# Performance work log

Hardware: AMD Instinct MI355X
Metric: run time of the kernel (lower is better)

## Reference

```python
import jax, jax.numpy as jnp
import numpy as np

B, L, M, H, VN, VK = 128, 30, 10, 256, 32000, 2000
VT = VN + VK


def setup_inputs() -> dict:
    key = jax.random.key(0)
    ks = jax.random.split(key, 24)
    p = lambda k, shape: jax.random.normal(k, shape, jnp.float32) * 0.02
    eye = jnp.eye(H, dtype=jnp.float32)
    return {
        "sentence": jax.random.randint(ks[0], (B, L, 1), 0, VN),
        "keywords": jax.random.randint(ks[1], (B, M, 1), VN, VT),
        "categories": jax.random.randint(ks[2], (B, M, 1), VN, VT),
        "memory_size": jax.random.randint(ks[3], (B,), 1, M + 1),
        "use_teacher_forcing": 1,
        "emb": p(ks[4], (VT, H)),
        "W_ct": p(ks[5], (H, 5 * H)), "b_ct": jnp.zeros((H,), jnp.float32),
        "W_ih": p(ks[6], (4 * H, H)), "W_hh": p(ks[7], (4 * H, H)),
        "b_ih": jnp.zeros((4 * H,), jnp.float32), "b_hh": jnp.zeros((4 * H,), jnp.float32),
        "W_n": eye + p(ks[8], (H, H)), "W_k": eye + p(ks[9], (H, H)), "W_v": eye + p(ks[10], (H, H)),
        "W_nv": p(ks[11], (VN, H)), "b_nv": jnp.zeros((VN,), jnp.float32),
        "W_g": p(ks[12], (1, H)), "b_g": jnp.zeros((1,), jnp.float32),
        "W_hn": p(ks[13], (L, (L + 1) * H)), "b_hn": jnp.zeros((L,), jnp.float32),
        "W_hk": p(ks[14], (L, (L + 1) * H)), "b_hk": jnp.zeros((L,), jnp.float32),
        "W_hv": p(ks[15], (L, (L + 1) * H)), "b_hv": jnp.zeros((L,), jnp.float32),
        "W_mk": p(ks[16], (M, 4 * H)), "b_mk": jnp.zeros((M,), jnp.float32),
        "W_mv": p(ks[17], (M, 4 * H)), "b_mv": jnp.zeros((M,), jnp.float32),
    }


def _forward(sentence, keywords, categories, memory_size, use_teacher_forcing,
             emb, W_ct, b_ct, W_ih, W_hh, b_ih, b_hh, W_n, W_k, W_v,
             W_nv, b_nv, W_g, b_g, W_hn, b_hn, W_hk, b_hk, W_hv, b_hv,
             W_mk, b_mk, W_mv, b_mv):
    # prepare_memory: embed keyword/category ids, zero rows past memory_size
    ke = emb[keywords[:, :, 0]]      # (B,M,H)
    ve = emb[categories[:, :, 0]]    # (B,M,H)
    mask = (jnp.arange(M)[None, :] < memory_size[:, None])[..., None].astype(emb.dtype)
    key_mem = ke * mask
    val_mem = ve * mask
    ms = memory_size.astype(emb.dtype)[:, None]
    # prepare_history: initial hidden = (avg_mk + avg_mv)/2 at t=0
    init_h = (key_mem.sum(1) + val_mem.sum(1)) / (2.0 * ms)  # (B,H)
    hist0 = jnp.zeros((B, L, H), emb.dtype).at[:, 0, :].set(init_h)

    toks = sentence[:, 1:, 0].T          # (L-1, B) teacher tokens
    dis = jnp.arange(1, L)

    def step(carry, xs):
        histN, histK, histV, prev_h, prev_emb, loss = carry
        di, tok = xs

        def attn_h(hist, W, b):
            q = jnp.concatenate([prev_h, hist.reshape(B, -1)], axis=1)  # (B,(L+1)H)
            w = jnp.tanh(q @ W.T + b)                                    # (B,L)
            return jnp.einsum('bl,blh->bh', w, hist)

        cHN = attn_h(histN, W_hn, b_hn)
        cHK = attn_h(histK, W_hk, b_hk)
        cHV = attn_h(histV, W_hv, b_hv)
        cH = jnp.concatenate([cHN, cHK, cHV], axis=1)  # (B,3H)
        q_m = jnp.concatenate([prev_h, cH], axis=1)    # (B,4H)

        def attn_m(mem, W, b):
            w = jnp.tanh(q_m @ W.T + b)                # (B,M)
            return jnp.einsum('bm,bmh->bh', w, mem)

        cMK = attn_m(key_mem, W_mk, b_mk)
        cMV = attn_m(val_mem, W_mv, b_mv)
        # W_Ct_reshape(cat 5H) -> LSTM initial cell state
        c0 = jnp.concatenate([cH, cMK, cMV], axis=1) @ W_ct.T + b_ct  # (B,H)
        # single-step LSTM (torch gate order i,f,g,o)
        gates = prev_emb @ W_ih.T + b_ih + prev_h @ W_hh.T + b_hh
        gi, gf, gg, go = jnp.split(gates, 4, axis=1)
        c = jax.nn.sigmoid(gf) * c0 + jax.nn.sigmoid(gi) * jnp.tanh(gg)
        h = jax.nn.sigmoid(go) * jnp.tanh(c)           # (B,H)

        hN = h @ W_n.T
        hK = h @ W_k.T
        hV = h @ W_v.T
        histN = histN.at[:, di, :].set(hN)
        histK = histK.at[:, di, :].set(hK)
        histV = histV.at[:, di, :].set(hV)

        P_N = jax.nn.softmax(hN @ W_nv.T + b_nv, axis=1)                       # (B,VN)
        P_MK = jax.nn.softmax(jnp.einsum('bmh,bh->bm', key_mem, hK), axis=1)   # (B,M)
        P_MV = jax.nn.softmax(jnp.einsum('bmh,bh->bm', val_mem, hV), axis=1)
        P_M = 0.5 * (P_MK + P_MV)
        gt = jax.nn.sigmoid(h @ W_g.T + b_g)           # (B,1)
        P = jnp.concatenate([P_N * gt, P_M * (1.0 - gt)], axis=1)
        p_tok = jnp.take_along_axis(P, tok[:, None], axis=1)[:, 0]
        loss = loss - jnp.log(p_tok).sum()
        prev_emb = emb[tok]                            # teacher forcing
        return (histN, histK, histV, h, prev_emb, loss), gt

    carry0 = (hist0, hist0, hist0, init_h, emb[sentence[:, 0, 0]],
              jnp.zeros((), emb.dtype))
    carry, gs = jax.lax.scan(step, carry0, (dis, toks))
    loss = carry[5]
    g_history = jnp.zeros((B, L, 1), emb.dtype).at[:, 1:, :].set(
        jnp.transpose(gs, (1, 0, 2)))
    return loss, g_history


def reference(sentence, keywords, categories, memory_size, use_teacher_forcing,
              emb, W_ct, b_ct, W_ih, W_hh, b_ih, b_hh, W_n, W_k, W_v,
              W_nv, b_nv, W_g, b_g, W_hn, b_hn, W_hk, b_hk, W_hv, b_hv,
              W_mk, b_mk, W_mv, b_mv):
    return _forward(sentence, keywords, categories, memory_size, use_teacher_forcing,
                    emb, W_ct, b_ct, W_ih, W_hh, b_ih, b_hh, W_n, W_k, W_v,
                    W_nv, b_nv, W_g, b_g, W_hn, b_hn, W_hk, b_hk, W_hv, b_hv,
                    W_mk, b_mk, W_mv, b_mv)
```

## Files before the change

### kernel.cpp

```cpp
#include <hip/hip_runtime.h>
#include <math.h>

#define B_ 128
#define L_ 30
#define M_ 10
#define H_ 256
#define VN_ 32000
#define NCHK 500
#define NG 3712

typedef __bf16 bf16;
typedef bf16 bf16x8 __attribute__((ext_vector_type(8)));
typedef float f32x4 __attribute__((ext_vector_type(4)));

#define MFMA(a,b,c) __builtin_amdgcn_mfma_f32_16x16x32_bf16(a, b, c, 0, 0, 0)

__device__ __forceinline__ float rcpf(float x) { return __builtin_amdgcn_rcpf(x); }
__device__ __forceinline__ float sigf(float x) { return rcpf(1.f + __expf(-x)); }
__device__ __forceinline__ float ftanh(float x) {
  float e = __expf(2.f * x);
  return 1.f - 2.f * rcpf(e + 1.f);
}
__device__ __forceinline__ float u2lo(unsigned w) { return __builtin_bit_cast(float, w << 16); }
__device__ __forceinline__ float u2hi(unsigned w) { return __builtin_bit_cast(float, w & 0xffff0000u); }
__device__ __forceinline__ unsigned packbf2(float a, float b) {
  unsigned short lo = __builtin_bit_cast(unsigned short, (bf16)a);
  unsigned short hi = __builtin_bit_cast(unsigned short, (bf16)b);
  return (unsigned)lo | ((unsigned)hi << 16);
}

#if __has_builtin(__builtin_amdgcn_fdot2_f32_bf16)
typedef __bf16 bf16x2 __attribute__((ext_vector_type(2)));
__device__ __forceinline__ float dot2(unsigned x, unsigned w, float c) {
  return __builtin_amdgcn_fdot2_f32_bf16(__builtin_bit_cast(bf16x2, x),
                                         __builtin_bit_cast(bf16x2, w), c, false);
}
#else
__device__ __forceinline__ float dot2(unsigned x, unsigned w, float c) {
  c = fmaf(u2lo(x), u2lo(w), c);
  return fmaf(u2hi(x), u2hi(w), c);
}
#endif

__global__ __launch_bounds__(256) void k_prep(
    const float* W_ct, const float* W_hh,
    const float* W_n, const float* W_k, const float* W_v,
    const float* W_hn, const float* W_hk, const float* W_hv,
    const float* W_mk, const float* W_mv, const float* W_g,
    unsigned* WhhP, unsigned* WnkvP, unsigned* WctPH, unsigned* WctP45,
    unsigned* WmP0, unsigned* WmPQ, unsigned* WhdA, unsigned* WhdB, unsigned* WgP) {
  int stride = gridDim.x * blockDim.x;
  int base = blockIdx.x * blockDim.x + threadIdx.x;
  for (int i = base; i < 131072; i += stride) {
    int k2 = i >> 10, n = i & 1023;
    WhhP[i] = packbf2(W_hh[n*256 + 2*k2], W_hh[n*256 + 2*k2 + 1]);
  }
  for (int i = base; i < 98304; i += stride) {
    int k2 = i / 768, n = i - (i/768)*768;
    const float* s = (n < 256) ? W_n : (n < 512) ? W_k : W_v;
    int nn = n & 255;
    WnkvP[i] = packbf2(s[nn*256 + 2*k2], s[nn*256 + 2*k2 + 1]);
  }
  for (int i = base; i < 98304; i += stride) {
    int X = i >> 15, r = i & 32767, k2 = r >> 8, n = r & 255;
    int col = X*256 + 2*k2;
    WctPH[i] = packbf2(W_ct[n*1280 + col], W_ct[n*1280 + col + 1]);
  }
  for (int i = base; i < 65536; i += stride) {
    int X = i >> 15, r = i & 32767, k2 = r >> 8, n = r & 255;
    int col = 768 + X*256 + 2*k2;
    WctP45[i] = packbf2(W_ct[n*1280 + col], W_ct[n*1280 + col + 1]);
  }
  for (int i = base; i < 4096; i += stride) {
    int k2 = i >> 5, c = i & 31;
    float x0 = 0.f, x1 = 0.f;
    if (c < 10)              { x0 = W_mk[c*1024 + 2*k2]; x1 = W_mk[c*1024 + 2*k2 + 1]; }
    else if (c >= 16 && c < 26) { int m = c-16; x0 = W_mv[m*1024 + 2*k2]; x1 = W_mv[m*1024 + 2*k2 + 1]; }
    WmP0[i] = packbf2(x0, x1);
  }
  for (int i = base; i < 12288; i += stride) {
    int X = i >> 12, r = i & 4095, k2 = r >> 5, c = r & 31;
    int off = 256 + X*256 + 2*k2;
    float x0 = 0.f, x1 = 0.f;
    if (c < 10)              { x0 = W_mk[c*1024 + off]; x1 = W_mk[c*1024 + off + 1]; }
    else if (c >= 16 && c < 26) { int m = c-16; x0 = W_mv[m*1024 + off]; x1 = W_mv[m*1024 + off + 1]; }
    WmPQ[i] = packbf2(x0, x1);
  }
  for (int i = base; i < 491520; i += stride) {
    int d = i >> 14, r = i & 16383, k2 = r >> 7, c = r & 127;
    float x0 = 0.f, x1 = 0.f;
    if (c < 96) {
      int X = c >> 5, l = c & 31;
      if (l < 30) {
        const float* W = (X == 0) ? W_hn : (X == 1) ? W_hk : W_hv;
        x0 = W[l*7936 + d*256 + 2*k2]; x1 = W[l*7936 + d*256 + 2*k2 + 1];
      }
    }
    WhdA[i] = packbf2(x0, x1);
  }
  for (int i = base; i < 16384; i += stride) {
    int k2 = i >> 7, c = i & 127;
    float x0 = 0.f, x1 = 0.f;
    if (c < 96) {
      int X = c >> 5, l = c & 31;
      if (l < 30) {
        const float* W = (X == 0) ? W_hn : (X == 1) ? W_hk : W_hv;
        x0 = W[l*7936 + 2*k2]; x1 = W[l*7936 + 2*k2 + 1];
      }
    }
    WhdB[i] = packbf2(x0, x1);
  }
  for (int i = base; i < 128; i += stride) WgP[i] = packbf2(W_g[2*i], W_g[2*i+1]);
}

__global__ __launch_bounds__(256) void k_pregates(
    const int* sentence, const float* emb, const float* W_ih,
    const float* b_ih, const float* b_hh, float* prehg) {
  extern __shared__ char smp[];
  char* Al = smp;
  char* Bl = smp + 65536;
  __shared__ int tok_s[128];
  int blk = blockIdx.x;
  int gd = blk >> 3, nc = blk & 7;
  int t = threadIdx.x, wid = t >> 6, lane = t & 63;
  if (t < 128) tok_s[t] = sentence[t*L_ + gd];
  __syncthreads();
  for (int i = t; i < 128*32; i += 256) {
    int r = i >> 5, c8 = i & 31;
    const float* e = emb + (size_t)tok_s[r]*H_ + c8*8;
    float4 f0 = *(const float4*)e, f1 = *(const float4*)(e + 4);
    int4 v;
    v.x = (int)packbf2(f0.x, f0.y); v.y = (int)packbf2(f0.z, f0.w);
    v.z = (int)packbf2(f1.x, f1.y); v.w = (int)packbf2(f1.z, f1.w);
    *(int4*)(Al + ((r*512 + c8*16) ^ ((r&7)<<4))) = v;
    const float* wsrc = W_ih + (size_t)(nc*128 + r)*H_ + c8*8;
    float4 g0 = *(const float4*)wsrc, g1 = *(const float4*)(wsrc + 4);
    int4 w;
    w.x = (int)packbf2(g0.x, g0.y); w.y = (int)packbf2(g0.z, g0.w);
    w.z = (int)packbf2(g1.x, g1.y); w.w = (int)packbf2(g1.z, g1.w);
    *(int4*)(Bl + ((r*512 + c8*16) ^ ((r&7)<<4))) = w;
  }
  __syncthreads();
  f32x4 acc[2][8] = {};
  #pragma unroll 2
  for (int kk = 0; kk < 8; ++kk) {
    int kb2 = kk*64 + (lane>>4)*16;
    bf16x8 af[2], bfr[8];
    #pragma unroll
    for (int fi = 0; fi < 2; ++fi) {
      int m = wid*32 + fi*16 + (lane & 15);
      af[fi] = *(const bf16x8*)(Al + ((m*512 + kb2) ^ ((m&7)<<4)));
    }
    #pragma unroll
    for (int fj = 0; fj < 8; ++fj) {
      int n = fj*16 + (lane & 15);
      bfr[fj] = *(const bf16x8*)(Bl + ((n*512 + kb2) ^ ((n&7)<<4)));
    }
    #pragma unroll
    for (int fi = 0; fi < 2; ++fi)
      #pragma unroll
      for (int fj = 0; fj < 8; ++fj)
        acc[fi][fj] = MFMA(af[fi], bfr[fj], acc[fi][fj]);
  }
  #pragma unroll
  for (int fi = 0; fi < 2; ++fi)
    #pragma unroll
    for (int fj = 0; fj < 8; ++fj)
      #pragma unroll
      for (int r = 0; r < 4; ++r) {
        int row = wid*32 + fi*16 + (lane>>4)*4 + r;
        int col = nc*128 + fj*16 + (lane & 15);
        prehg[((size_t)gd*128 + row)*1024 + col] = acc[fi][fj][r] + b_ih[col] + b_hh[col];
      }
}

struct LoopP {
  const int *sentence, *keywords, *categories, *memsz;
  const float *emb;
  const unsigned *WhhP, *WnkvP, *WctPH, *WctP45, *WmP0, *WmPQ, *WhdA, *WhdB, *WgP;
  const float *prehg;
  const float *b_ct, *b_hn, *b_hk, *b_hv, *b_mk, *b_mv, *b_g;
  unsigned* hNb;
  unsigned* hNbT;
  float* gt_all;
  float* outg;
};

__global__ __launch_bounds__(1024) void k_loop(LoopP p) {
  extern __shared__ unsigned Su[];
  float* Sf = (float*)Su;
  const int t = threadIdx.x, b = blockIdx.x;
  enum { PH = 0,
         QM = 11520,
         P45 = 14400,
         MB = 16960,
         GA = 19520,
         HP = 20544,
         HV = 20672,
         SW = 21056, ACA = 21152, SWM = 21248, M0 = 21280,
         DA = 21312, DB = 21440,
         BCT = 21568, BH = 21824, BM = 21920, BG = 21952 };

  for (int i = t; i < 2560; i += 1024) {
    int X = i / 1280, r = i - X*1280, m = r >> 7, j = r & 127;
    int ms = p.memsz[b];
    int idx = (X == 0 ? p.keywords : p.categories)[b*M_ + m];
    unsigned u = 0;
    if (m < ms) {
      const float* e = p.emb + (size_t)idx*H_ + 2*j;
      u = packbf2(e[0], e[1]);
    }
    Su[MB + i] = u;
  }
  if (t < 256) Sf[BCT + t] = p.b_ct[t];
  if (t < 96) {
    int X = t >> 5, l = t & 31;
    const float* bh = (X == 0) ? p.b_hn : (X == 1) ? p.b_hk : p.b_hv;
    Sf[BH + t] = (l < 30) ? bh[l] : 0.f;
    Sf[ACA + t] = 0.f;
  }
  if (t < 32) {
    float v = 0.f;
    if (t < 10) v = p.b_mk[t];
    else if (t >= 16 && t < 26) v = p.b_mv[t - 16];
    Sf[BM + t] = v;
  }
  if (t == 0) { Sf[BG] = p.b_g[0]; p.outg[b*L_] = 0.f; }
  __syncthreads();
  if (t < 128) {
    float a0 = 0.f, a1 = 0.f;
    #pragma unroll
    for (int q = 0; q < 20; ++q) {
      unsigned u = Su[MB + q*128 + t];
      a0 += u2lo(u); a1 += u2hi(u);
    }
    float msf = (float)p.memsz[b];
    unsigned up = packbf2(a0 / (2.f * msf), a1 / (2.f * msf));
    Su[HP + t] = up;
    Su[HV + t] = up; Su[HV + 128 + t] = up; Su[HV + 256 + t] = up;
  }
  for (int q = t; q < 2560; q += 1024) {
    int X = q / 1280, r = q - X*1280, m = r >> 7, j = r & 127;
    float a0 = 0.f, a1 = 0.f;
    const uint2* wp = (const uint2*)(p.WctP45 + (X << 15)) + j;
    const unsigned* mb = Su + MB + X*1280 + m*128;
    #pragma unroll 4
    for (int k2 = 0; k2 < 128; ++k2) {
      uint2 w = wp[k2 << 7];
      unsigned u = mb[k2];
      a0 = dot2(u, w.x, a0);
      a1 = dot2(u, w.y, a1);
    }
    Su[P45 + q] = packbf2(a0, a1);
  }
  __syncthreads();

  for (int di = 1; di < L_; ++di) {
    {
      const float pre = p.prehg[(size_t)(((di-1) << 7) | b)*1024 + t];
      float e0 = 0.f, e1 = 0.f;
      const unsigned* wp = p.WhhP + t;
      #pragma unroll 8
      for (int k2 = 0; k2 < 128; k2 += 2) {
        e0 = dot2(Su[HP + k2],     wp[k2 << 10],     e0);
        e1 = dot2(Su[HP + k2 + 1], wp[(k2+1) << 10], e1);
      }
      Sf[GA + t] = pre + e0 + e1;
    }
    if (t < 128) {
      float a = 0.f;
      const unsigned* wp = p.WhdA + ((size_t)di << 14) + t;
      const unsigned* hv = Su + HV + ((t >> 5) << 7);
      #pragma unroll 8
      for (int k2 = 0; k2 < 128; ++k2) a = dot2(hv[k2 & 127], wp[k2 << 7], a);
      Sf[DA + t] = a;
    } else if (t < 256) {
      int c = t - 128;
      float a = 0.f;
      const unsigned* wp = p.WhdB + c;
      #pragma unroll 8
      for (int k2 = 0; k2 < 128; ++k2) a = dot2(Su[HP + k2], wp[k2 << 7], a);
      Sf[DB + c] = a;
    } else if (t < 640) {
      int q = t - 256, X = q >> 7, j = q & 127;
      float a0 = 0.f, a1 = 0.f;
      const unsigned* hv = Su + HV + (X << 7);
      const uint2* wp = (const uint2*)(p.WctPH + (X << 15)) + j;
      #pragma unroll 4
      for (int k2 = 0; k2 < 128; ++k2) {
        uint2 w = wp[k2 << 7];
        a0 = dot2(hv[k2], w.x, a0);
        a1 = dot2(hv[k2], w.y, a1);
      }
      Su[PH + (X*30 + di-1)*128 + j] = packbf2(a0, a1);
    } else if (t < 736) {
      int q = t - 640, X = q >> 5, c = q & 31;
      float a = 0.f;
      const unsigned* wp = p.WmPQ + (X << 12) + c;
      const unsigned* hv = Su + HV + (X << 7);
      #pragma unroll 8
      for (int k2 = 0; k2 < 128; ++k2) a = dot2(hv[k2], wp[k2 << 5], a);
      Sf[QM + (X*30 + di-1)*32 + c] = a;
    } else if (t >= 768 && t < 800) {
      int c = t - 768;
      float a = 0.f;
      const unsigned* wp = p.WmP0 + c;
      #pragma unroll 8
      for (int k2 = 0; k2 < 128; ++k2) a = dot2(Su[HP + k2], wp[k2 << 5], a);
      Sf[M0 + c] = a;
    }
    __syncthreads();
    if (t < 96) {
      float a = Sf[ACA + t] + Sf[DA + t];
      Sf[ACA + t] = a;
      Sf[SW + t] = ftanh(a + Sf[DB + t] + Sf[BH + t]);
    }
    __syncthreads();
    if (t < 32) {
      bool valid = (t < 10) || (t >= 16 && t < 26);
      if (valid) {
        float aN = 0.f, aK = 0.f, aV = 0.f;
        const float* sw0 = Sf + SW;
        const float* q0 = Sf + QM + t;
        for (int l = 0; l < di; ++l) {
          aN = fmaf(sw0[l],      q0[l*32],        aN);
          aK = fmaf(sw0[32 + l], q0[960 + l*32],  aK);
          aV = fmaf(sw0[64 + l], q0[1920 + l*32], aV);
        }
        Sf[SWM + t] = ftanh(Sf[M0 + t] + Sf[BM + t] + aN + aK + aV);
      }
    }
    __syncthreads();
    if (t < 128) {
      float a0 = Sf[BCT + 2*t], a1 = Sf[BCT + 2*t + 1];
      for (int X = 0; X < 3; ++X) {
        const float* swp = Sf + SW + X*32;
        const unsigned* php = Su + PH + X*3840 + t;
        float e0 = 0.f, e1 = 0.f, o0 = 0.f, o1 = 0.f;
        int l = 0;
        for (; l + 1 < di; l += 2) {
          float s0 = swp[l], s1 = swp[l+1];
          unsigned ua = php[l*128], ub = php[(l+1)*128];
          e0 = fmaf(s0, u2lo(ua), e0); e1 = fmaf(s0, u2hi(ua), e1);
          o0 = fmaf(s1, u2lo(ub), o0); o1 = fmaf(s1, u2hi(ub), o1);
        }
        if (l < di) {
          float s = swp[l]; unsigned u = php[l*128];
          e0 = fmaf(s, u2lo(u), e0); e1 = fmaf(s, u2hi(u), e1);
        }
        a0 += e0 + o0; a1 += e1 + o1;
      }
      {
        float p0 = 0.f, p1 = 0.f, q0 = 0.f, q1 = 0.f;
        #pragma unroll
        for (int m = 0; m < 10; ++m) {
          float sk = Sf[SWM + m], sv = Sf[SWM + 16 + m];
          unsigned uk = Su[P45 + m*128 + t], uv = Su[P45 + 1280 + m*128 + t];
          p0 = fmaf(sk, u2lo(uk), p0); p1 = fmaf(sk, u2hi(uk), p1);
          q0 = fmaf(sv, u2lo(uv), q0); q1 = fmaf(sv, u2hi(uv), q1);
        }
        a0 += p0 + q0; a1 += p1 + q1;
      }
      int n0 = 2*t;
      float gi0 = Sf[GA+n0],   gf0 = Sf[GA+256+n0], gg0 = Sf[GA+512+n0], go0 = Sf[GA+768+n0];
      float gi1 = Sf[GA+n0+1], gf1 = Sf[GA+257+n0], gg1 = Sf[GA+513+n0], go1 = Sf[GA+769+n0];
      float cc0 = sigf(gf0)*a0 + sigf(gi0)*ftanh(gg0);
      float cc1 = sigf(gf1)*a1 + sigf(gi1)*ftanh(gg1);
      float h0 = sigf(go0)*ftanh(cc0);
      float h1 = sigf(go1)*ftanh(cc1);
      Su[HP + t] = packbf2(h0, h1);
    }
    __syncthreads();
    if (t < 384) {
      int X = t >> 7, j = t & 127;
      float a0 = 0.f, a1 = 0.f;
      const uint2* wp = (const uint2*)p.WnkvP + t;
      #pragma unroll 4
      for (int k2 = 0; k2 < 128; ++k2) {
        uint2 w = wp[k2*384];
        unsigned u = Su[HP + k2];
        a0 = dot2(u, w.x, a0);
        a1 = dot2(u, w.y, a1);
      }
      unsigned up = packbf2(a0, a1);
      Su[HV + t] = up;
      if (X == 0) {
        int tile = di - 1;
        p.hNb[(size_t)((tile << 7) | b)*128 + j] = up;
        int idx = ((((tile*4 + (b>>5))*8 + (j>>4))*64 + ((j>>2)&3)*16 + (b&15))*2 + ((b>>4)&1))*4 + (j&3);
        p.hNbT[idx] = up;
      }
    } else if (t >= 448 && t < 512) {
      int j = t - 448;
      float a = dot2(Su[HP + 2*j], p.WgP[2*j], 0.f);
      a = dot2(Su[HP + 2*j + 1], p.WgP[2*j + 1], a);
      #pragma unroll
      for (int o = 1; o < 64; o <<= 1) a += __shfl_xor(a, o);
      if (j == 0) {
        float g = sigf(a + Sf[BG]);
        p.gt_all[((di-1) << 7) | b] = g;
        p.outg[b*L_ + di] = g;
      }
    }
    __syncthreads();
  }
}

__global__ __launch_bounds__(256) void k_vocab(
    const unsigned* hNbT, const float* W_nv, const float* b_nv, float2* pmps) {
  extern __shared__ char smv[];
  int ch = blockIdx.x;
  int t = threadIdx.x, wid = t >> 6, lane = t & 63;
  int v0 = ch * 64;
  for (int i = t; i < 64*32; i += 256) {
    int r = i >> 5, c8 = i & 31;
    const float* wsrc = W_nv + (size_t)(v0 + r)*H_ + c8*8;
    float4 f0 = *(const float4*)wsrc, f1 = *(const float4*)(wsrc + 4);
    int4 v;
    v.x = (int)packbf2(f0.x, f0.y); v.y = (int)packbf2(f0.z, f0.w);
    v.z = (int)packbf2(f1.x, f1.y); v.w = (int)packbf2(f1.z, f1.w);
    *(int4*)(smv + ((r*512 + c8*16) ^ ((r&7)<<4))) = v;
  }
  float bb4[4];
  #pragma unroll
  for (int fj = 0; fj < 4; ++fj) bb4[fj] = b_nv[v0 + fj*16 + (lane & 15)];
  __syncthreads();
  const int4* At = (const int4*)hNbT;
  for (int tile = 0; tile < 29; ++tile) {
    f32x4 acc[2][4] = {};
    #pragma unroll 2
    for (int kk = 0; kk < 8; ++kk) {
      int kb2 = kk*64 + (lane>>4)*16;
      bf16x8 af[2], bfr[4];
      #pragma unroll
      for (int fi = 0; fi < 2; ++fi) {
        int4 u = At[((tile*4 + wid)*8 + kk)*128 + lane*2 + fi];
        af[fi] = __builtin_bit_cast(bf16x8, u);
      }
      #pragma unroll
      for (int fj = 0; fj < 4; ++fj) {
        int n = fj*16 + (lane & 15);
        bfr[fj] = *(const bf16x8*)(smv + ((n*512 + kb2) ^ ((n&7)<<4)));
      }
      #pragma unroll
      for (int fi = 0; fi < 2; ++fi)
        #pragma unroll
        for (int fj = 0; fj < 4; ++fj)
          acc[fi][fj] = MFMA(af[fi], bfr[fj], acc[fi][fj]);
    }
    #pragma unroll
    for (int fi = 0; fi < 2; ++fi)
      #pragma unroll
      for (int r = 0; r < 4; ++r) {
        float mi = acc[fi][0][r] + bb4[0];
        #pragma unroll
        for (int fj = 1; fj < 4; ++fj) mi = fmaxf(mi, acc[fi][fj][r] + bb4[fj]);
        for (int o = 1; o < 16; o <<= 1) mi = fmaxf(mi, __shfl_xor(mi, o));
        float si = 0.f;
        #pragma unroll
        for (int fj = 0; fj < 4; ++fj) si += __expf(acc[fi][fj][r] + bb4[fj] - mi);
        for (int o = 1; o < 16; o <<= 1) si += __shfl_xor(si, o);
        if ((lane & 15) == 0) {
          int row = wid*32 + fi*16 + (lane>>4)*4 + r;
          pmps[(size_t)ch*NG + tile*128 + row] = make_float2(mi, si);
        }
      }
  }
}

__global__ __launch_bounds__(128) void k_combine(
    const float2* pmps, const unsigned* hNb, const float* W_nv, const float* b_nv,
    const float* gt_all, const int* sentence, float* loss_part) {
  __shared__ float red[128];
  int tile = blockIdx.x, bb = threadIdx.x;
  int g = tile*128 + bb;
  float M = -1e30f, Ssum = 0.f;
  for (int c = 0; c < NCHK; ++c) {
    float2 v = pmps[(size_t)c*NG + g];
    float M2 = fmaxf(M, v.x);
    Ssum = Ssum*__expf(M - M2) + v.y*__expf(v.x - M2);
    M = M2;
  }
  int tok = sentence[bb*L_ + tile + 1];
  float z = b_nv[tok];
  const unsigned* hu = hNb + (size_t)g*128;
  const float* wr = W_nv + (size_t)tok*H_;
  #pragma unroll 8
  for (int k = 0; k < 128; ++k) {
    unsigned w2 = hu[k];
    z += u2lo(w2)*wr[2*k] + u2hi(w2)*wr[2*k + 1];
  }
  float term = -(z - M - __logf(Ssum) + __logf(gt_all[g]));
  red[bb] = term;
  __syncthreads();
  for (int o = 64; o > 0; o >>= 1) {
    if (bb < o) red[bb] += red[bb + o];
    __syncthreads();
  }
  if (bb == 0) loss_part[tile] = red[0];
}

__global__ __launch_bounds__(64) void k_fin(const float* lp, float* out) {
  int t = threadIdx.x;
  float v = (t < 29) ? lp[t] : 0.f;
  for (int o = 1; o < 64; o <<= 1) v += __shfl_xor(v, o);
  if (t == 0) out[0] = v;
}

extern "C" void kernel_launch(void* const* d_in, const int* in_sizes, int n_in,
                              void* d_out, int out_size, void* d_ws, size_t ws_size,
                              hipStream_t stream) {
  const int* sentence  = (const int*)d_in[0];
  const int* keywords  = (const int*)d_in[1];
  const int* categories= (const int*)d_in[2];
  const int* memsz     = (const int*)d_in[3];
  const float* emb  = (const float*)d_in[5];
  const float* W_ct = (const float*)d_in[6];
  const float* b_ct = (const float*)d_in[7];
  const float* W_ih = (const float*)d_in[8];
  const float* W_hh = (const float*)d_in[9];
  const float* b_ih = (const float*)d_in[10];
  const float* b_hh = (const float*)d_in[11];
  const float* W_n  = (const float*)d_in[12];
  const float* W_k  = (const float*)d_in[13];
  const float* W_v  = (const float*)d_in[14];
  const float* W_nv = (const float*)d_in[15];
  const float* b_nv = (const float*)d_in[16];
  const float* W_g  = (const float*)d_in[17];
  const float* b_g  = (const float*)d_in[18];
  const float* W_hn = (const float*)d_in[19];
  const float* b_hn = (const float*)d_in[20];
  const float* W_hk = (const float*)d_in[21];
  const float* b_hk = (const float*)d_in[22];
  const float* W_hv = (const float*)d_in[23];
  const float* b_hv = (const float*)d_in[24];
  const float* W_mk = (const float*)d_in[25];
  const float* b_mk = (const float*)d_in[26];
  const float* W_mv = (const float*)d_in[27];
  const float* b_mv = (const float*)d_in[28];
  float* out = (float*)d_out;

  char* wsp = (char*)d_ws;
  size_t off = 0;
  auto alloc = [&](size_t bytes) -> void* {
    void* pp = wsp + off;
    off = (off + bytes + 255) & ~(size_t)255;
    return pp;
  };
  unsigned* WhhP   = (unsigned*)alloc((size_t)131072*4);
  unsigned* WnkvP  = (unsigned*)alloc((size_t)98304*4);
  unsigned* WctPH  = (unsigned*)alloc((size_t)98304*4);
  unsigned* WctP45 = (unsigned*)alloc((size_t)65536*4);
  unsigned* WmP0   = (unsigned*)alloc((size_t)4096*4);
  unsigned* WmPQ   = (unsigned*)alloc((size_t)12288*4);
  unsigned* WhdA   = (unsigned*)alloc((size_t)491520*4);
  unsigned* WhdB   = (unsigned*)alloc((size_t)16384*4);
  unsigned* WgP    = (unsigned*)alloc((size_t)128*4);
  float* prehg     = (float*)alloc((size_t)29*B_*1024*4);
  unsigned* hNb    = (unsigned*)alloc((size_t)29*B_*128*4);
  unsigned* hNbT   = (unsigned*)alloc((size_t)29*B_*128*4);
  float* gt_all    = (float*)alloc((size_t)29*B_*4);
  float2* pmps     = (float2*)alloc((size_t)NCHK*NG*8);
  float* loss_part = (float*)alloc(29*4);

  k_prep<<<512, 256, 0, stream>>>(W_ct, W_hh, W_n, W_k, W_v,
      W_hn, W_hk, W_hv, W_mk, W_mv, W_g,
      WhhP, WnkvP, WctPH, WctP45, WmP0, WmPQ, WhdA, WhdB, WgP);
  k_pregates<<<232, 256, 131072, stream>>>(sentence, emb, W_ih, b_ih, b_hh, prehg);

  LoopP P;
  P.sentence = sentence; P.keywords = keywords; P.categories = categories; P.memsz = memsz;
  P.emb = emb;
  P.WhhP = WhhP; P.WnkvP = WnkvP; P.WctPH = WctPH; P.WctP45 = WctP45;
  P.WmP0 = WmP0; P.WmPQ = WmPQ; P.WhdA = WhdA; P.WhdB = WhdB; P.WgP = WgP;
  P.prehg = prehg;
  P.b_ct = b_ct; P.b_hn = b_hn; P.b_hk = b_hk; P.b_hv = b_hv;
  P.b_mk = b_mk; P.b_mv = b_mv; P.b_g = b_g;
  P.hNb = hNb; P.hNbT = hNbT; P.gt_all = gt_all; P.outg = out + 1;

  k_loop<<<B_, 1024, 87812, stream>>>(P);
  k_vocab<<<NCHK, 256, 32768, stream>>>(hNbT, W_nv, b_nv, pmps);
  k_combine<<<29, 128, 0, stream>>>(pmps, hNb, W_nv, b_nv, gt_all, sentence, loss_part);
  k_fin<<<1, 64, 0, stream>>>(loss_part, out);
}
```

Measured before the change: 821.0 us.

## Repack recurrent weights for 16-byte loads with split-K shuffle reduction

The weight matrices used in the serial recurrent loop are repacked so each thread issues 128-bit loads covering four outputs for a slice of K. Groups of four lanes then combine their partial sums with xor shuffles, cutting the number of global load instructions per step. Separately, the vocab kernel keeps its B fragments in registers across all tiles instead of reloading them from LDS. The partial max/sum buffer is transposed so the combine kernel reads contiguously. The cost is more register pressure, extra shuffles, and a more complex packing scheme in the prep kernel.

```diff
diff --git a/kernel.cpp b/kernel.cpp
--- a/kernel.cpp
+++ b/kernel.cpp
@@ -47,47 +47,55 @@
     const float* W_n, const float* W_k, const float* W_v,
     const float* W_hn, const float* W_hk, const float* W_hv,
     const float* W_mk, const float* W_mv, const float* W_g,
-    unsigned* WhhP, unsigned* WnkvP, unsigned* WctPH, unsigned* WctP45,
-    unsigned* WmP0, unsigned* WmPQ, unsigned* WhdA, unsigned* WhdB, unsigned* WgP) {
+    unsigned* W4g, unsigned* W4nkv, unsigned* W4ph, unsigned* WctP45,
+    unsigned* W4m0, unsigned* W4qm, unsigned* W4da, unsigned* W4db, unsigned* WgP) {
   int stride = gridDim.x * blockDim.x;
   int base = blockIdx.x * blockDim.x + threadIdx.x;
-  for (int i = base; i < 131072; i += stride) {
-    int k2 = i >> 10, n = i & 1023;
-    WhhP[i] = packbf2(W_hh[n*256 + 2*k2], W_hh[n*256 + 2*k2 + 1]);
-  }
-  for (int i = base; i < 98304; i += stride) {
-    int k2 = i / 768, n = i - (i/768)*768;
-    const float* s = (n < 256) ? W_n : (n < 512) ? W_k : W_v;
+  for (int idx = base; idx < 131072; idx += stride) {
+    int s = idx & 3, tt = (idx >> 2) & 1023, i = idx >> 12;
+    int n = 4*(tt >> 2) + s, k2 = (tt & 3) + 4*i;
+    W4g[idx] = packbf2(W_hh[n*256 + 2*k2], W_hh[n*256 + 2*k2 + 1]);
+  }
+  for (int idx = base; idx < 98304; idx += stride) {
+    int s = idx & 3, r2 = idx >> 2, tt = r2 % 384, i = r2 / 384;
+    int n = 4*(tt >> 1) + s, k2 = (tt & 1) + 2*i;
+    const float* src = (n < 256) ? W_n : (n < 512) ? W_k : W_v;
     int nn = n & 255;
-    WnkvP[i] = packbf2(s[nn*256 + 2*k2], s[nn*256 + 2*k2 + 1]);
-  }
-  for (int i = base; i < 98304; i += stride) {
-    int X = i >> 15, r = i & 32767, k2 = r >> 8, n = r & 255;
+    W4nkv[idx] = packbf2(src[nn*256 + 2*k2], src[nn*256 + 2*k2 + 1]);
+  }
+  for (int idx = base; idx < 98304; idx += stride) {
+    int s = idx & 3, r2 = idx >> 2, q = r2 % 384, i = r2 / 384;
+    int X = q >> 7, r = q & 127, j2 = r >> 1, kh = r & 1;
+    int nl = 4*j2 + s, k2 = kh + 2*i;
     int col = X*256 + 2*k2;
-    WctPH[i] = packbf2(W_ct[n*1280 + col], W_ct[n*1280 + col + 1]);
+    W4ph[idx] = packbf2(W_ct[nl*1280 + col], W_ct[nl*1280 + col + 1]);
   }
   for (int i = base; i < 65536; i += stride) {
     int X = i >> 15, r = i & 32767, k2 = r >> 8, n = r & 255;
     int col = 768 + X*256 + 2*k2;
     WctP45[i] = packbf2(W_ct[n*1280 + col], W_ct[n*1280 + col + 1]);
   }
-  for (int i = base; i < 4096; i += stride) {
-    int k2 = i >> 5, c = i & 31;
+  for (int idx = base; idx < 4096; idx += stride) {
+    int s = idx & 3, tt = (idx >> 2) & 31, i = idx >> 7;
+    int c = 4*(tt >> 2) + s, k2 = (tt & 3) + 4*i;
     float x0 = 0.f, x1 = 0.f;
     if (c < 10)              { x0 = W_mk[c*1024 + 2*k2]; x1 = W_mk[c*1024 + 2*k2 + 1]; }
     else if (c >= 16 && c < 26) { int m = c-16; x0 = W_mv[m*1024 + 2*k2]; x1 = W_mv[m*1024 + 2*k2 + 1]; }
-    WmP0[i] = packbf2(x0, x1);
-  }
-  for (int i = base; i < 12288; i += stride) {
-    int X = i >> 12, r = i & 4095, k2 = r >> 5, c = r & 31;
+    W4m0[idx] = packbf2(x0, x1);
+  }
+  for (int idx = base; idx < 12288; idx += stride) {
+    int s = idx & 3, r2 = idx >> 2, q = r2 % 96, i = r2 / 96;
+    int X = q >> 5, r = q & 31;
+    int c = 4*(r >> 2) + s, k2 = (r & 3) + 4*i;
     int off = 256 + X*256 + 2*k2;
     float x0 = 0.f, x1 = 0.f;
     if (c < 10)              { x0 = W_mk[c*1024 + off]; x1 = W_mk[c*1024 + off + 1]; }
     else if (c >= 16 && c < 26) { int m = c-16; x0 = W_mv[m*1024 + off]; x1 = W_mv[m*1024 + off + 1]; }
-    WmPQ[i] = packbf2(x0, x1);
-  }
-  for (int i = base; i < 491520; i += stride) {
-    int d = i >> 14, r = i & 16383, k2 = r >> 7, c = r & 127;
+    W4qm[idx] = packbf2(x0, x1);
+  }
+  for (int idx = base; idx < 491520; idx += stride) {
+    int s = idx & 3, tt = (idx >> 2) & 127, i = (idx >> 9) & 31, d = idx >> 14;
+    int c = 4*(tt >> 2) + s, k2 = (tt & 3) + 4*i;
     float x0 = 0.f, x1 = 0.f;
     if (c < 96) {
       int X = c >> 5, l = c & 31;
@@ -96,10 +104,11 @@
         x0 = W[l*7936 + d*256 + 2*k2]; x1 = W[l*7936 + d*256 + 2*k2 + 1];
       }
     }
-    WhdA[i] = packbf2(x0, x1);
-  }
-  for (int i = base; i < 16384; i += stride) {
-    int k2 = i >> 7, c = i & 127;
+    W4da[idx] = packbf2(x0, x1);
+  }
+  for (int idx = base; idx < 16384; idx += stride) {
+    int s = idx & 3, tt = (idx >> 2) & 127, i = idx >> 9;
+    int c = 4*(tt >> 2) + s, k2 = (tt & 3) + 4*i;
     float x0 = 0.f, x1 = 0.f;
     if (c < 96) {
       int X = c >> 5, l = c & 31;
@@ -108,7 +117,7 @@
         x0 = W[l*7936 + 2*k2]; x1 = W[l*7936 + 2*k2 + 1];
       }
     }
-    WhdB[i] = packbf2(x0, x1);
+    W4db[idx] = packbf2(x0, x1);
   }
   for (int i = base; i < 128; i += stride) WgP[i] = packbf2(W_g[2*i], W_g[2*i+1]);
 }
@@ -177,7 +186,7 @@
 struct LoopP {
   const int *sentence, *keywords, *categories, *memsz;
   const float *emb;
-  const unsigned *WhhP, *WnkvP, *WctPH, *WctP45, *WmP0, *WmPQ, *WhdA, *WhdB, *WgP;
+  const unsigned *W4g, *W4nkv, *W4ph, *WctP45, *W4m0, *W4qm, *W4da, *W4db, *WgP;
   const float *prehg;
   const float *b_ct, *b_hn, *b_hk, *b_hv, *b_mk, *b_mv, *b_g;
   unsigned* hNb;
@@ -190,13 +199,8 @@
   extern __shared__ unsigned Su[];
   float* Sf = (float*)Su;
   const int t = threadIdx.x, b = blockIdx.x;
-  enum { PH = 0,
-         QM = 11520,
-         P45 = 14400,
-         MB = 16960,
-         GA = 19520,
-         HP = 20544,
-         HV = 20672,
+  enum { PH = 0, QM = 11520, P45 = 14400, MB = 16960,
+         GA = 19520, HP = 20544, HV = 20672,
          SW = 21056, ACA = 21152, SWM = 21248, M0 = 21280,
          DA = 21312, DB = 21440,
          BCT = 21568, BH = 21824, BM = 21920, BG = 21952 };
@@ -258,56 +262,102 @@
   for (int di = 1; di < L_; ++di) {
     {
       const float pre = p.prehg[(size_t)(((di-1) << 7) | b)*1024 + t];
-      float e0 = 0.f, e1 = 0.f;
-      const unsigned* wp = p.WhhP + t;
+      int kq = t & 3;
+      const uint4* wr = (const uint4*)p.W4g + t;
+      const unsigned* xp = Su + HP + kq;
+      float p0 = 0.f, p1 = 0.f, p2 = 0.f, p3 = 0.f;
       #pragma unroll 8
-      for (int k2 = 0; k2 < 128; k2 += 2) {
-        e0 = dot2(Su[HP + k2],     wp[k2 << 10],     e0);
-        e1 = dot2(Su[HP + k2 + 1], wp[(k2+1) << 10], e1);
-      }
-      Sf[GA + t] = pre + e0 + e1;
+      for (int i = 0; i < 32; ++i) {
+        uint4 w = wr[(size_t)i << 10];
+        unsigned x = xp[4*i];
+        p0 = dot2(x, w.x, p0); p1 = dot2(x, w.y, p1);
+        p2 = dot2(x, w.z, p2); p3 = dot2(x, w.w, p3);
+      }
+      p0 += __shfl_xor(p0, 1); p1 += __shfl_xor(p1, 1); p2 += __shfl_xor(p2, 1); p3 += __shfl_xor(p3, 1);
+      p0 += __shfl_xor(p0, 2); p1 += __shfl_xor(p1, 2); p2 += __shfl_xor(p2, 2); p3 += __shfl_xor(p3, 2);
+      float sel = (kq == 0) ? p0 : (kq == 1) ? p1 : (kq == 2) ? p2 : p3;
+      Sf[GA + t] = pre + sel;
     }
     if (t < 128) {
-      float a = 0.f;
-      const unsigned* wp = p.WhdA + ((size_t)di << 14) + t;
-      const unsigned* hv = Su + HV + ((t >> 5) << 7);
+      int kq = t & 3;
+      const uint4* wr = (const uint4*)p.W4da + (size_t)di*4096 + t;
+      const unsigned* xp = Su + HV + ((t >> 5) << 7) + kq;
+      float p0 = 0.f, p1 = 0.f, p2 = 0.f, p3 = 0.f;
       #pragma unroll 8
-      for (int k2 = 0; k2 < 128; ++k2) a = dot2(hv[k2 & 127], wp[k2 << 7], a);
-      Sf[DA + t] = a;
+      for (int i = 0; i < 32; ++i) {
+        uint4 w = wr[i << 7];
+        unsigned x = xp[4*i];
+        p0 = dot2(x, w.x, p0); p1 = dot2(x, w.y, p1);
+        p2 = dot2(x, w.z, p2); p3 = dot2(x, w.w, p3);
+      }
+      p0 += __shfl_xor(p0, 1); p1 += __shfl_xor(p1, 1); p2 += __shfl_xor(p2, 1); p3 += __shfl_xor(p3, 1);
+      p0 += __shfl_xor(p0, 2); p1 += __shfl_xor(p1, 2); p2 += __shfl_xor(p2, 2); p3 += __shfl_xor(p3, 2);
+      float sel = (kq == 0) ? p0 : (kq == 1) ? p1 : (kq == 2) ? p2 : p3;
+      Sf[DA + t] = sel;
     } else if (t < 256) {
-      int c = t - 128;
-      float a = 0.f;
-      const unsigned* wp = p.WhdB + c;
+      int c = t - 128, kq = c & 3;
+      const uint4* wr = (const uint4*)p.W4db + c;
+      const unsigned* xp = Su + HP + kq;
+      float p0 = 0.f, p1 = 0.f, p2 = 0.f, p3 = 0.f;
       #pragma unroll 8
-      for (int k2 = 0; k2 < 128; ++k2) a = dot2(Su[HP + k2], wp[k2 << 7], a);
-      Sf[DB + c] = a;
+      for (int i = 0; i < 32; ++i) {
+        uint4 w = wr[i << 7];
+        unsigned x = xp[4*i];
+        p0 = dot2(x, w.x, p0); p1 = dot2(x, w.y, p1);
+        p2 = dot2(x, w.z, p2); p3 = dot2(x, w.w, p3);
+      }
+      p0 += __shfl_xor(p0, 1); p1 += __shfl_xor(p1, 1); p2 += __shfl_xor(p2, 1); p3 += __shfl_xor(p3, 1);
+      p0 += __shfl_xor(p0, 2); p1 += __shfl_xor(p1, 2); p2 += __shfl_xor(p2, 2); p3 += __shfl_xor(p3, 2);
+      float sel = (kq == 0) ? p0 : (kq == 1) ? p1 : (kq == 2) ? p2 : p3;
+      Sf[DB + c] = sel;
     } else if (t < 640) {
-      int q = t - 256, X = q >> 7, j = q & 127;
-      float a0 = 0.f, a1 = 0.f;
-      const unsigned* hv = Su + HV + (X << 7);
-      const uint2* wp = (const uint2*)(p.WctPH + (X << 15)) + j;
-      #pragma unroll 4
-      for (int k2 = 0; k2 < 128; ++k2) {
-        uint2 w = wp[k2 << 7];
-        a0 = dot2(hv[k2], w.x, a0);
-        a1 = dot2(hv[k2], w.y, a1);
-      }
-      Su[PH + (X*30 + di-1)*128 + j] = packbf2(a0, a1);
+      int q = t - 256;
+      int X = q >> 7, r = q & 127, kh = r & 1;
+      const uint4* wr = (const uint4*)p.W4ph + q;
+      const unsigned* xp = Su + HV + (X << 7) + kh;
+      float p0 = 0.f, p1 = 0.f, p2 = 0.f, p3 = 0.f;
+      #pragma unroll 8
+      for (int i = 0; i < 64; ++i) {
+        uint4 w = wr[i*384];
+        unsigned x = xp[2*i];
+        p0 = dot2(x, w.x, p0); p1 = dot2(x, w.y, p1);
+        p2 = dot2(x, w.z, p2); p3 = dot2(x, w.w, p3);
+      }
+      p0 += __shfl_xor(p0, 1); p1 += __shfl_xor(p1, 1); p2 += __shfl_xor(p2, 1); p3 += __shfl_xor(p3, 1);
+      unsigned val = kh ? packbf2(p2, p3) : packbf2(p0, p1);
+      Su[PH + (X*30 + di-1)*128 + r] = val;
     } else if (t < 736) {
-      int q = t - 640, X = q >> 5, c = q & 31;
-      float a = 0.f;
-      const unsigned* wp = p.WmPQ + (X << 12) + c;
-      const unsigned* hv = Su + HV + (X << 7);
+      int q = t - 640, X = q >> 5, r = q & 31, kq = r & 3;
+      const uint4* wr = (const uint4*)p.W4qm + q;
+      const unsigned* xp = Su + HV + (X << 7) + kq;
+      float p0 = 0.f, p1 = 0.f, p2 = 0.f, p3 = 0.f;
       #pragma unroll 8
-      for (int k2 = 0; k2 < 128; ++k2) a = dot2(hv[k2], wp[k2 << 5], a);
-      Sf[QM + (X*30 + di-1)*32 + c] = a;
+      for (int i = 0; i < 32; ++i) {
+        uint4 w = wr[i*96];
+        unsigned x = xp[4*i];
+        p0 = dot2(x, w.x, p0); p1 = dot2(x, w.y, p1);
+        p2 = dot2(x, w.z, p2); p3 = dot2(x, w.w, p3);
+      }
+      p0 += __shfl_xor(p0, 1); p1 += __shfl_xor(p1, 1); p2 += __shfl_xor(p2, 1); p3 += __shfl_xor(p3, 1);
+      p0 += __shfl_xor(p0, 2); p1 += __shfl_xor(p1, 2); p2 += __shfl_xor(p2, 2); p3 += __shfl_xor(p3, 2);
+      float sel = (kq == 0) ? p0 : (kq == 1) ? p1 : (kq == 2) ? p2 : p3;
+      Sf[QM + (X*30 + di-1)*32 + r] = sel;
     } else if (t >= 768 && t < 800) {
-      int c = t - 768;
-      float a = 0.f;
-      const unsigned* wp = p.WmP0 + c;
+      int r = t - 768, kq = r & 3;
+      const uint4* wr = (const uint4*)p.W4m0 + r;
+      const unsigned* xp = Su + HP + kq;
+      float p0 = 0.f, p1 = 0.f, p2 = 0.f, p3 = 0.f;
       #pragma unroll 8
-      for (int k2 = 0; k2 < 128; ++k2) a = dot2(Su[HP + k2], wp[k2 << 5], a);
-      Sf[M0 + c] = a;
+      for (int i = 0; i < 32; ++i) {
+        uint4 w = wr[i << 5];
+        unsigned x = xp[4*i];
+        p0 = dot2(x, w.x, p0); p1 = dot2(x, w.y, p1);
+        p2 = dot2(x, w.z, p2); p3 = dot2(x, w.w, p3);
+      }
+      p0 += __shfl_xor(p0, 1); p1 += __shfl_xor(p1, 1); p2 += __shfl_xor(p2, 1); p3 += __shfl_xor(p3, 1);
+      p0 += __shfl_xor(p0, 2); p1 += __shfl_xor(p1, 2); p2 += __shfl_xor(p2, 2); p3 += __shfl_xor(p3, 2);
+      float sel = (kq == 0) ? p0 : (kq == 1) ? p1 : (kq == 2) ? p2 : p3;
+      Sf[M0 + r] = sel;
     }
     __syncthreads();
     if (t < 96) {
@@ -372,18 +422,21 @@
     }
     __syncthreads();
     if (t < 384) {
+      int kh = t & 1;
+      const uint4* wr = (const uint4*)p.W4nkv + t;
+      const unsigned* xp = Su + HP + kh;
+      float p0 = 0.f, p1 = 0.f, p2 = 0.f, p3 = 0.f;
+      #pragma unroll 8
+      for (int i = 0; i < 64; ++i) {
+        uint4 w = wr[i*384];
+        unsigned x = xp[2*i];
+        p0 = dot2(x, w.x, p0); p1 = dot2(x, w.y, p1);
+        p2 = dot2(x, w.z, p2); p3 = dot2(x, w.w, p3);
+      }
+      p0 += __shfl_xor(p0, 1); p1 += __shfl_xor(p1, 1); p2 += __shfl_xor(p2, 1); p3 += __shfl_xor(p3, 1);
+      unsigned up = kh ? packbf2(p2, p3) : packbf2(p0, p1);
+      Su[HV + t] = up;
       int X = t >> 7, j = t & 127;
-      float a0 = 0.f, a1 = 0.f;
-      const uint2* wp = (const uint2*)p.WnkvP + t;
-      #pragma unroll 4
-      for (int k2 = 0; k2 < 128; ++k2) {
-        uint2 w = wp[k2*384];
-        unsigned u = Su[HP + k2];
-        a0 = dot2(u, w.x, a0);
-        a1 = dot2(u, w.y, a1);
-      }
-      unsigned up = packbf2(a0, a1);
-      Su[HV + t] = up;
       if (X == 0) {
         int tile = di - 1;
         p.hNb[(size_t)((tile << 7) | b)*128 + j] = up;
@@ -425,28 +478,32 @@
   #pragma unroll
   for (int fj = 0; fj < 4; ++fj) bb4[fj] = b_nv[v0 + fj*16 + (lane & 15)];
   __syncthreads();
+  bf16x8 Breg[8][4];
+  #pragma unroll
+  for (int kk = 0; kk < 8; ++kk) {
+    int kb2 = kk*64 + (lane>>4)*16;
+    #pragma unroll
+    for (int fj = 0; fj < 4; ++fj) {
+      int n = fj*16 + (lane & 15);
+      Breg[kk][fj] = *(const bf16x8*)(smv + ((n*512 + kb2) ^ ((n&7)<<4)));
+    }
+  }
   const int4* At = (const int4*)hNbT;
   for (int tile = 0; tile < 29; ++tile) {
     f32x4 acc[2][4] = {};
-    #pragma unroll 2
+    #pragma unroll
     for (int kk = 0; kk < 8; ++kk) {
-      int kb2 = kk*64 + (lane>>4)*16;
-      bf16x8 af[2], bfr[4];
+      bf16x8 af[2];
       #pragma unroll
       for (int fi = 0; fi < 2; ++fi) {
         int4 u = At[((tile*4 + wid)*8 + kk)*128 + lane*2 + fi];
         af[fi] = __builtin_bit_cast(bf16x8, u);
       }
       #pragma unroll
-      for (int fj = 0; fj < 4; ++fj) {
-        int n = fj*16 + (lane & 15);
-        bfr[fj] = *(const bf16x8*)(smv + ((n*512 + kb2) ^ ((n&7)<<4)));
-      }
-      #pragma unroll
       for (int fi = 0; fi < 2; ++fi)
         #pragma unroll
         for (int fj = 0; fj < 4; ++fj)
-          acc[fi][fj] = MFMA(af[fi], bfr[fj], acc[fi][fj]);
+          acc[fi][fj] = MFMA(af[fi], Breg[kk][fj], acc[fi][fj]);
     }
     #pragma unroll
     for (int fi = 0; fi < 2; ++fi)
@@ -462,7 +519,7 @@
         for (int o = 1; o < 16; o <<= 1) si += __shfl_xor(si, o);
         if ((lane & 15) == 0) {
           int row = wid*32 + fi*16 + (lane>>4)*4 + r;
-          pmps[(size_t)ch*NG + tile*128 + row] = make_float2(mi, si);
+          pmps[(size_t)(tile*128 + row)*512 + ch] = make_float2(mi, si);
         }
       }
   }
@@ -475,8 +532,10 @@
   int tile = blockIdx.x, bb = threadIdx.x;
   int g = tile*128 + bb;
   float M = -1e30f, Ssum = 0.f;
+  const float2* pv = pmps + (size_t)g*512;
+  #pragma unroll 4
   for (int c = 0; c < NCHK; ++c) {
-    float2 v = pmps[(size_t)c*NG + g];
+    float2 v = pv[c];
     float M2 = fmaxf(M, v.x);
     Ssum = Ssum*__expf(M - M2) + v.y*__expf(v.x - M2);
     M = M2;
@@ -547,32 +606,32 @@
     off = (off + bytes + 255) & ~(size_t)255;
     return pp;
   };
-  unsigned* WhhP   = (unsigned*)alloc((size_t)131072*4);
-  unsigned* WnkvP  = (unsigned*)alloc((size_t)98304*4);
-  unsigned* WctPH  = (unsigned*)alloc((size_t)98304*4);
+  unsigned* W4g    = (unsigned*)alloc((size_t)131072*4);
+  unsigned* W4nkv  = (unsigned*)alloc((size_t)98304*4);
+  unsigned* W4ph   = (unsigned*)alloc((size_t)98304*4);
   unsigned* WctP45 = (unsigned*)alloc((size_t)65536*4);
-  unsigned* WmP0   = (unsigned*)alloc((size_t)4096*4);
-  unsigned* WmPQ   = (unsigned*)alloc((size_t)12288*4);
-  unsigned* WhdA   = (unsigned*)alloc((size_t)491520*4);
-  unsigned* WhdB   = (unsigned*)alloc((size_t)16384*4);
+  unsigned* W4m0   = (unsigned*)alloc((size_t)4096*4);
+  unsigned* W4qm   = (unsigned*)alloc((size_t)12288*4);
+  unsigned* W4da   = (unsigned*)alloc((size_t)491520*4);
+  unsigned* W4db   = (unsigned*)alloc((size_t)16384*4);
   unsigned* WgP    = (unsigned*)alloc((size_t)128*4);
   float* prehg     = (float*)alloc((size_t)29*B_*1024*4);
   unsigned* hNb    = (unsigned*)alloc((size_t)29*B_*128*4);
   unsigned* hNbT   = (unsigned*)alloc((size_t)29*B_*128*4);
   float* gt_all    = (float*)alloc((size_t)29*B_*4);
-  float2* pmps     = (float2*)alloc((size_t)NCHK*NG*8);
+  float2* pmps     = (float2*)alloc((size_t)NG*512*8);
   float* loss_part = (float*)alloc(29*4);
 
   k_prep<<<512, 256, 0, stream>>>(W_ct, W_hh, W_n, W_k, W_v,
       W_hn, W_hk, W_hv, W_mk, W_mv, W_g,
-      WhhP, WnkvP, WctPH, WctP45, WmP0, WmPQ, WhdA, WhdB, WgP);
+      W4g, W4nkv, W4ph, WctP45, W4m0, W4qm, W4da, W4db, WgP);
   k_pregates<<<232, 256, 131072, stream>>>(sentence, emb, W_ih, b_ih, b_hh, prehg);
 
   LoopP P;
   P.sentence = sentence; P.keywords = keywords; P.categories = categories; P.memsz = memsz;
   P.emb = emb;
-  P.WhhP = WhhP; P.WnkvP = WnkvP; P.WctPH = WctPH; P.WctP45 = WctP45;
-  P.WmP0 = WmP0; P.WmPQ = WmPQ; P.WhdA = WhdA; P.WhdB = WhdB; P.WgP = WgP;
+  P.W4g = W4g; P.W4nkv = W4nkv; P.W4ph = W4ph; P.WctP45 = WctP45;
+  P.W4m0 = W4m0; P.W4qm = W4qm; P.W4da = W4da; P.W4db = W4db; P.WgP = WgP;
   P.prehg = prehg;
   P.b_ct = b_ct; P.b_hn = b_hn; P.b_hk = b_hk; P.b_hv = b_hv;
   P.b_mk = b_mk; P.b_mv = b_mv; P.b_g = b_g;
```

Result: faster. 659.5 us (-19.7%).
